# Kernel tuning notes

Hardware: AMD Instinct MI355X
Metric: run time of the kernel (lower is better)

Reference implementation:

```python
import jax, jax.numpy as jnp
import numpy as np

NUM_HEADS = 8
EMBED_DIM = 512
EXPAND = 3
RPE_DIM = 512
RPE_LAYERS = 3
B, N = 4, 2048
D1 = (EXPAND * EMBED_DIM) // NUM_HEADS * NUM_HEADS  # 1536
HEAD_DIM = D1 // NUM_HEADS  # 192


def srms(x):
    # SimpleRMSNorm: x / (||x||_2 * d^{-1/2} + eps)
    d = x.shape[-1]
    rms = jnp.linalg.norm(x, axis=-1, keepdims=True) * (d ** -0.5)
    return x / (rms + 1e-8)


def rpe_net(idx, Wp, bp, Wl, bl, Wr, br):
    # idx: (m, 1) relative positions -> (m, h*head_dim)
    h = idx @ Wp.T + bp
    for i in range(Wl.shape[0]):  # fixed small layer count
        h = jax.nn.relu(srms(h)) @ Wl[i].T + bl[i]
    return jax.nn.relu(srms(h)) @ Wr.T + br


def setup_inputs() -> dict:
    key = jax.random.key(0)
    ks = jax.random.split(key, 12)
    s = 0.02
    return {
        "x": jax.random.normal(ks[0], (B, N, EMBED_DIM), jnp.float32),
        "Wu": jax.random.normal(ks[1], (D1, EMBED_DIM), jnp.float32) * s,
        "bu": jnp.zeros((D1,), jnp.float32),
        "Wv": jax.random.normal(ks[2], (D1, EMBED_DIM), jnp.float32) * s,
        "bv": jnp.zeros((D1,), jnp.float32),
        "Wo": jax.random.normal(ks[3], (EMBED_DIM, D1), jnp.float32) * s,
        "bo": jnp.zeros((EMBED_DIM,), jnp.float32),
        "Wp": jax.random.normal(ks[4], (RPE_DIM, 1), jnp.float32) * s,
        "bp": jax.random.normal(ks[5], (RPE_DIM,), jnp.float32) * s,
        "Wl": jax.random.normal(ks[6], (RPE_LAYERS, RPE_DIM, RPE_DIM), jnp.float32) * s,
        "bl": jax.random.normal(ks[7], (RPE_LAYERS, RPE_DIM), jnp.float32) * s,
        "Wr": jax.random.normal(ks[8], (NUM_HEADS * HEAD_DIM, RPE_DIM), jnp.float32) * s,
        "br": jax.random.normal(ks[9], (NUM_HEADS * HEAD_DIM,), jnp.float32) * s,
    }


def reference(x, Wu, bu, Wv, bv, Wo, bo, Wp, bp, Wl, bl, Wr, br):
    b, n, e = x.shape
    d1 = Wu.shape[0]
    hd = d1 // NUM_HEADS
    u = jax.nn.silu(x @ Wu.T + bu)                       # (b, n, d1)
    v = jax.nn.silu(x @ Wv.T + bv)                       # (b, n, d1)
    v = v.reshape(b, n, NUM_HEADS, hd).transpose(0, 2, 1, 3)  # (b, h, n, d)
    # Tno non-causal, par_type=1: indices [0, 1..n-1, 0, -(n-1)..-1]
    pos = jnp.arange(1, n, dtype=x.dtype)
    zero = jnp.zeros((1,), x.dtype)
    idx = jnp.concatenate([zero, pos, zero, -pos[::-1]])[:, None]  # (2n, 1)
    a = rpe_net(idx, Wp, bp, Wl, bl, Wr, br)             # (2n, h*d)
    a = a.reshape(2 * n, NUM_HEADS, hd).transpose(1, 0, 2)  # (h, 2n, d)
    m = 2 * n
    # circular conv of length 2n along sequence, truncate to n
    y = jnp.fft.rfft(v, m, axis=2) * jnp.fft.rfft(a, m, axis=1)[None]
    out = jnp.fft.irfft(y, m, axis=2)[:, :, :n, :]       # (b, h, n, d)
    out = out.transpose(0, 2, 1, 3).reshape(b, n, d1)    # (b, n, d1)
    return (u * out) @ Wo.T + bo
```

## Files before the change

### kernel.cpp

```cpp
#include <hip/hip_runtime.h>

#define N_SEQ 2048
#define M_FFT 4096
#define D1    1536
#define NH    8
#define HD    192
#define ED    512

typedef __bf16 bf16;
typedef __bf16 bf16x2 __attribute__((ext_vector_type(2)));
typedef __bf16 bf16x4 __attribute__((ext_vector_type(4)));
typedef __bf16 bf16x8 __attribute__((ext_vector_type(8)));
typedef float  floatx4 __attribute__((ext_vector_type(4)));

enum { MODE_PLAIN = 0, MODE_SILU_VT = 2, MODE_AT = 3 };

__device__ __forceinline__ void gload16(const void* g, void* l) {
    __builtin_amdgcn_global_load_lds(
        (const __attribute__((address_space(1))) void*)g,
        (__attribute__((address_space(3))) void*)l, 16, 0, 0);
}

template<int MODE, typename OutT>
__global__ __launch_bounds__(256) void gemm_bf16(
    const bf16* __restrict__ A, const bf16* __restrict__ Bw,
    const float* __restrict__ bias, OutT* __restrict__ C,
    int M, int Nc, int K)
{
    __shared__ __align__(16) bf16 As[128 * 32];
    __shared__ __align__(16) bf16 Bs[128 * 32];

    const int tid  = threadIdx.x;
    const int row0 = blockIdx.y * 128;
    const int col0 = blockIdx.x * 128;
    const int wid  = tid >> 6;
    const int lane = tid & 63;
    const int lm   = lane & 15;
    const int lk   = lane >> 4;
    const int wm   = wid >> 1;
    const int wn   = wid & 1;
    const int ldrow  = tid >> 2;
    const int ldcol8 = (tid & 3) * 8;

    floatx4 acc[4][4] = {};

    const bf16* Ag = A  + ((size_t)(row0 + ldrow)) * K + ldcol8;
    const bf16* Bg = Bw + ((size_t)(col0 + ldrow)) * K + ldcol8;
    bf16* AsW = As + (wid * 16) * 32;
    bf16* BsW = Bs + (wid * 16) * 32;

    for (int k0 = 0; k0 < K; k0 += 32) {
        gload16(Ag + k0, AsW);
        gload16(Ag + (size_t)64 * K + k0, AsW + 64 * 32);
        gload16(Bg + k0, BsW);
        gload16(Bg + (size_t)64 * K + k0, BsW + 64 * 32);
        __syncthreads();

        bf16x8 af[4], bfr[4];
        #pragma unroll
        for (int mi = 0; mi < 4; ++mi)
            af[mi] = *(const bf16x8*)&As[(wm * 64 + mi * 16 + lm) * 32 + lk * 8];
        #pragma unroll
        for (int nj = 0; nj < 4; ++nj)
            bfr[nj] = *(const bf16x8*)&Bs[(wn * 64 + nj * 16 + lm) * 32 + lk * 8];
        #pragma unroll
        for (int mi = 0; mi < 4; ++mi)
            #pragma unroll
            for (int nj = 0; nj < 4; ++nj)
                acc[mi][nj] = __builtin_amdgcn_mfma_f32_16x16x32_bf16(
                    af[mi], bfr[nj], acc[mi][nj], 0, 0, 0);
        __syncthreads();
    }

    float bcol[4];
    #pragma unroll
    for (int nj = 0; nj < 4; ++nj)
        bcol[nj] = bias[col0 + wn * 64 + nj * 16 + lm];

    #pragma unroll
    for (int mi = 0; mi < 4; ++mi) {
        const int rbase = row0 + wm * 64 + mi * 16 + lk * 4;
        #pragma unroll
        for (int nj = 0; nj < 4; ++nj) {
            const int col = col0 + wn * 64 + nj * 16 + lm;
            float vals[4];
            #pragma unroll
            for (int r = 0; r < 4; ++r) {
                float val = acc[mi][nj][r] + bcol[nj];
                if (MODE == MODE_SILU_VT)
                    val = val / (1.0f + __expf(-val));
                vals[r] = val;
            }
            if (MODE == MODE_SILU_VT) {
                int b = rbase >> 11, s = rbase & 2047;
                bf16x4 o;
                #pragma unroll
                for (int r = 0; r < 4; ++r) o[r] = (bf16)vals[r];
                *(bf16x4*)&((bf16*)C)[((size_t)(b * D1 + col)) * N_SEQ + s] = o;
            } else if (MODE == MODE_AT) {
                float4 o = make_float4(vals[0], vals[1], vals[2], vals[3]);
                *(float4*)&((float*)C)[(size_t)col * M + rbase] = o;
            } else {
                #pragma unroll
                for (int r = 0; r < 4; ++r)
                    C[(size_t)(rbase + r) * Nc + col] = (OutT)vals[r];
            }
        }
    }
}

__global__ __launch_bounds__(256) void f2b_kernel(
    const float* __restrict__ in, bf16* __restrict__ out, int n)
{
    int i = (blockIdx.x * 256 + threadIdx.x) * 4;
    if (i >= n) return;
    float4 f = *(const float4*)(in + i);
    union { bf16 h[4]; short4 s; } u4;
    u4.h[0] = (bf16)f.x; u4.h[1] = (bf16)f.y;
    u4.h[2] = (bf16)f.z; u4.h[3] = (bf16)f.w;
    *(short4*)(out + i) = u4.s;
}

__global__ __launch_bounds__(256) void f2b5_kernel(
    const float* __restrict__ s0, const float* __restrict__ s1,
    const float* __restrict__ s2, const float* __restrict__ s3,
    const float* __restrict__ s4, bf16* __restrict__ dst)
{
    const int seg = blockIdx.y;
    const float* src = seg == 0 ? s0 : seg == 1 ? s1 : seg == 2 ? s2
                     : seg == 3 ? s3 : s4;
    int i = (blockIdx.x * 256 + threadIdx.x) * 4;
    float4 f = *(const float4*)(src + i);
    union { bf16 h[4]; short4 s; } u4;
    u4.h[0] = (bf16)f.x; u4.h[1] = (bf16)f.y;
    u4.h[2] = (bf16)f.z; u4.h[3] = (bf16)f.w;
    *(short4*)(dst + (size_t)seg * 786432 + i) = u4.s;
}

__global__ __launch_bounds__(256) void rpe_in_srms_kernel(
    const float* __restrict__ Wp, const float* __restrict__ bp,
    bf16* __restrict__ g)
{
    const int j = blockIdx.x;
    const int tid = threadIdx.x;
    float idxv = (j < N_SEQ) ? (float)j
                             : (j == N_SEQ ? 0.0f : (float)(j - 2 * N_SEQ));
    float h1 = idxv * Wp[tid] + bp[tid];
    float h2 = idxv * Wp[tid + 256] + bp[tid + 256];
    float ss = h1 * h1 + h2 * h2;
    #pragma unroll
    for (int off = 32; off > 0; off >>= 1) ss += __shfl_down(ss, off, 64);
    __shared__ float red[4];
    if ((tid & 63) == 0) red[tid >> 6] = ss;
    __syncthreads();
    float tot = red[0] + red[1] + red[2] + red[3];
    float scale = 1.0f / (sqrtf(tot) * 0.04419417382415922f + 1e-8f);
    g[(size_t)j * ED + tid]       = (bf16)fmaxf(h1 * scale, 0.0f);
    g[(size_t)j * ED + tid + 256] = (bf16)fmaxf(h2 * scale, 0.0f);
}

__global__ __launch_bounds__(256) void srms_relu_kernel(
    const float* __restrict__ in, bf16* __restrict__ out)
{
    const int row = blockIdx.x;
    const int tid = threadIdx.x;
    const float* p = in + (size_t)row * ED;

    float ss = 0.0f;
    for (int i = tid; i < ED; i += 256) { float x = p[i]; ss += x * x; }
    #pragma unroll
    for (int off = 32; off > 0; off >>= 1) ss += __shfl_down(ss, off, 64);
    __shared__ float red[4];
    if ((tid & 63) == 0) red[tid >> 6] = ss;
    __syncthreads();
    float tot = red[0] + red[1] + red[2] + red[3];
    float scale = 1.0f / (sqrtf(tot) * 0.04419417382415922f + 1e-8f);
    for (int i = tid; i < ED; i += 256)
        out[(size_t)row * ED + i] = (bf16)fmaxf(p[i] * scale, 0.0f);
}

#define FFT_LDS_SZ 4381

__device__ __forceinline__ int fpad(int i) { return i + (i >> 4) + 2 * (i >> 8); }

__device__ __forceinline__ float2 cmul(float2 a, float2 b) {
    return make_float2(a.x * b.x - a.y * b.y, a.x * b.y + a.y * b.x);
}
__device__ __forceinline__ float2 cadd(float2 a, float2 b) {
    return make_float2(a.x + b.x, a.y + b.y);
}
__device__ __forceinline__ float2 csub(float2 a, float2 b) {
    return make_float2(a.x - b.x, a.y - b.y);
}
__host__ __device__ constexpr int brev4(int t) {
    return ((t & 1) << 3) | ((t & 2) << 1) | ((t & 4) >> 1) | ((t & 8) >> 3);
}

template<bool FWD>
__device__ __forceinline__ void w16_tab(float2 w[8]) {
    const float sg = FWD ? -1.0f : 1.0f;
    const float C1 = 0.9238795325112867f, S1 = 0.3826834323650898f;
    const float C2 = 0.7071067811865476f;
    w[0] = make_float2( 1.f, 0.f);
    w[1] = make_float2( C1, sg * S1);
    w[2] = make_float2( C2, sg * C2);
    w[3] = make_float2( S1, sg * C1);
    w[4] = make_float2(0.f, sg * 1.f);
    w[5] = make_float2(-S1, sg * C1);
    w[6] = make_float2(-C2, sg * C2);
    w[7] = make_float2(-C1, sg * S1);
}

__device__ __forceinline__ void fft16_dif_tail(float2 x[16], const float2 w[8]) {
    #pragma unroll
    for (int b = 0; b < 16; b += 8)
        #pragma unroll
        for (int k = 0; k < 4; ++k) {
            float2 u = x[b + k], t = x[b + k + 4];
            x[b + k] = cadd(u, t); x[b + k + 4] = cmul(csub(u, t), w[2 * k]);
        }
    #pragma unroll
    for (int b = 0; b < 16; b += 4)
        #pragma unroll
        for (int k = 0; k < 2; ++k) {
            float2 u = x[b + k], t = x[b + k + 2];
            x[b + k] = cadd(u, t); x[b + k + 2] = cmul(csub(u, t), w[4 * k]);
        }
    #pragma unroll
    for (int b = 0; b < 16; b += 2) {
        float2 u = x[b], t = x[b + 1];
        x[b] = cadd(u, t); x[b + 1] = csub(u, t);
    }
}

__device__ __forceinline__ void fft16_dif(float2 x[16]) {
    float2 w[8]; w16_tab<true>(w);
    #pragma unroll
    for (int k = 0; k < 8; ++k) {
        float2 u = x[k], t = x[k + 8];
        x[k] = cadd(u, t); x[k + 8] = cmul(csub(u, t), w[k]);
    }
    fft16_dif_tail(x, w);
}

__device__ __forceinline__ void fft16_dif_halfzero(float2 x[16]) {
    float2 w[8]; w16_tab<true>(w);
    x[8] = x[0];
    #pragma unroll
    for (int k = 1; k < 8; ++k) x[k + 8] = cmul(x[k], w[k]);
    fft16_dif_tail(x, w);
}

template<bool HALF_OUT>
__device__ __forceinline__ void fft16_dit_inv(float2 x[16]) {
    float2 w[8]; w16_tab<false>(w);
    #pragma unroll
    for (int b = 0; b < 16; b += 2) {
        float2 u = x[b], t = x[b + 1];
        x[b] = cadd(u, t); x[b + 1] = csub(u, t);
    }
    #pragma unroll
    for (int b = 0; b < 16; b += 4)
        #pragma unroll
        for (int k = 0; k < 2; ++k) {
            float2 u = x[b + k], t = cmul(x[b + k + 2], w[4 * k]);
            x[b + k] = cadd(u, t); x[b + k + 2] = csub(u, t);
        }
    #pragma unroll
    for (int b = 0; b < 16; b += 8)
        #pragma unroll
        for (int k = 0; k < 4; ++k) {
            float2 u = x[b + k], t = cmul(x[b + k + 4], w[2 * k]);
            x[b + k] = cadd(u, t); x[b + k + 4] = csub(u, t);
        }
    #pragma unroll
    for (int k = 0; k < 8; ++k) {
        float2 u = x[k], t = cmul(x[k + 8], w[k]);
        x[k] = cadd(u, t);
        if (!HALF_OUT) x[k + 8] = csub(u, t);
    }
}

__device__ __forceinline__ void stage_twiddle(float2 v[16], int j, float den, float sgn)
{
    float s, c;
    __sincosf(sgn * 6.283185307179586f * (float)j / den, &s, &c);
    float2 w1 = make_float2(c, s), wt = make_float2(1.f, 0.f);
    #pragma unroll
    for (int tau = 1; tau < 16; ++tau) {
        wt = cmul(wt, w1);
        v[brev4(tau)] = cmul(v[brev4(tau)], wt);
    }
}

template<bool HALF_ZERO>
__device__ void fft4096_fwd(float2* d, int tid)
{
    float2 v[16];
    {
        const int j = tid;
        if (HALF_ZERO) {
            #pragma unroll
            for (int t = 0; t < 8; ++t) v[t] = d[fpad(j + (t << 8))];
            fft16_dif_halfzero(v);
        } else {
            #pragma unroll
            for (int t = 0; t < 16; ++t) v[t] = d[fpad(j + (t << 8))];
            fft16_dif(v);
        }
        stage_twiddle(v, j, 4096.0f, -1.0f);
        #pragma unroll
        for (int p = 0; p < 16; ++p) d[fpad(j + (p << 8))] = v[p];
    }
    __syncthreads();
    {
        const int base = ((tid >> 4) << 8) + (tid & 15);
        #pragma unroll
        for (int t = 0; t < 16; ++t) v[t] = d[fpad(base + (t << 4))];
        fft16_dif(v);
        stage_twiddle(v, tid & 15, 256.0f, -1.0f);
        #pragma unroll
        for (int p = 0; p < 16; ++p) d[fpad(base + (p << 4))] = v[p];
    }
    __syncthreads();
    {
        const int base = tid << 4;
        #pragma unroll
        for (int t = 0; t < 16; ++t) v[t] = d[fpad(base + t)];
        fft16_dif(v);
        #pragma unroll
        for (int p = 0; p < 16; ++p) d[fpad(base + p)] = v[p];
    }
    __syncthreads();
}

template<bool HALF_OUT>
__device__ void fft4096_inv(float2* d, int tid)
{
    float2 v[16];
    {
        const int base = tid << 4;
        #pragma unroll
        for (int p = 0; p < 16; ++p) v[p] = d[fpad(base + p)];
        fft16_dit_inv<false>(v);
        #pragma unroll
        for (int t = 0; t < 16; ++t) d[fpad(base + t)] = v[t];
    }
    __syncthreads();
    {
        const int base = ((tid >> 4) << 8) + (tid & 15);
        #pragma unroll
        for (int p = 0; p < 16; ++p) v[p] = d[fpad(base + (p << 4))];
        stage_twiddle(v, tid & 15, 256.0f, 1.0f);
        fft16_dit_inv<false>(v);
        #pragma unroll
        for (int t = 0; t < 16; ++t) d[fpad(base + (t << 4))] = v[t];
    }
    __syncthreads();
    {
        const int j = tid;
        #pragma unroll
        for (int p = 0; p < 16; ++p) v[p] = d[fpad(j + (p << 8))];
        stage_twiddle(v, j, 4096.0f, 1.0f);
        fft16_dit_inv<HALF_OUT>(v);
        #pragma unroll
        for (int t = 0; t < (HALF_OUT ? 8 : 16); ++t) d[fpad(j + (t << 8))] = v[t];
    }
    __syncthreads();
}

__global__ __launch_bounds__(256) void fft_a_kernel(
    const float* __restrict__ a_t, float2* __restrict__ Wspec)
{
    __shared__ float2 data[FFT_LDS_SZ];
    const int tid = threadIdx.x;
    const int h = blockIdx.x / 96, dp = blockIdx.x % 96;

    const float* r0 = a_t + ((size_t)(h * HD + 2 * dp)) * M_FFT;
    const float* r1 = r0 + M_FFT;

    for (int j = tid; j < 4096; j += 256) data[fpad(j)] = make_float2(r0[j], r1[j]);
    __syncthreads();
    fft4096_fwd<false>(data, tid);

    float2* outrow = Wspec + (size_t)blockIdx.x * 4096;
    for (int j = tid; j < 4096; j += 256) outrow[j] = data[fpad(j)];
}

__global__ __launch_bounds__(256) void fft_conv_kernel(
    const bf16* __restrict__ v_t, const float2* __restrict__ Wspec,
    const bf16* __restrict__ u_t, bf16* __restrict__ gated_t)
{
    __shared__ float2 data[FFT_LDS_SZ];
    const int tid = threadIdx.x;
    const int bx = blockIdx.x;
    const int b  = bx / 768;
    const int r  = bx % 768;
    const int h  = r / 96, dp = r % 96;
    const int ch = h * HD + 2 * dp;

    const bf16* z0 = v_t + ((size_t)(b * D1 + ch)) * N_SEQ;
    const bf16* z1 = z0 + N_SEQ;

    {
        const int s = tid * 8;
        bf16x8 a0 = *(const bf16x8*)(z0 + s);
        bf16x8 a1 = *(const bf16x8*)(z1 + s);
        #pragma unroll
        for (int i = 0; i < 8; ++i)
            data[fpad(s + i)] = make_float2((float)a0[i], (float)a1[i]);
    }
    __syncthreads();

    fft4096_fwd<true>(data, tid);

    const float2* Wrow = Wspec + (size_t)r * 4096;
    for (int k = tid; k <= 2048; k += 256) {
        int km = (4096 - k) & 4095;
        int p1 = __brev((unsigned)k)  >> 20;
        int p2 = __brev((unsigned)km) >> 20;
        float2 Zk = data[fpad(p1)], Zm = data[fpad(p2)];
        float2 Wk = Wrow[p1], Wm = Wrow[p2];
        float2 V0 = make_float2(0.5f * (Zk.x + Zm.x), 0.5f * (Zk.y - Zm.y));
        float2 V1 = make_float2(0.5f * (Zk.y + Zm.y), 0.5f * (Zm.x - Zk.x));
        float2 A0 = make_float2(0.5f * (Wk.x + Wm.x), 0.5f * (Wk.y - Wm.y));
        float2 A1 = make_float2(0.5f * (Wk.y + Wm.y), 0.5f * (Wm.x - Wk.x));
        float2 P = make_float2(V0.x * A0.x - V0.y * A0.y, V0.x * A0.y + V0.y * A0.x);
        float2 Q = make_float2(V1.x * A1.x - V1.y * A1.y, V1.x * A1.y + V1.y * A1.x);
        data[fpad(p1)] = make_float2(P.x - Q.y, P.y + Q.x);
        if (k != 0 && k != 2048)
            data[fpad(p2)] = make_float2(P.x + Q.y, Q.x - P.y);
    }
    __syncthreads();

    fft4096_inv<true>(data, tid);

    const float inv_m = 1.0f / 4096.0f;
    const bf16* u0 = u_t + ((size_t)(b * D1 + ch)) * N_SEQ;
    const bf16* u1 = u0 + N_SEQ;
    bf16* g0 = gated_t + ((size_t)(b * D1 + ch)) * N_SEQ;
    bf16* g1 = g0 + N_SEQ;
    {
        const int t = tid * 8;
        bf16x8 ua = *(const bf16x8*)(u0 + t);
        bf16x8 ub = *(const bf16x8*)(u1 + t);
        bf16x8 oa, ob;
        #pragma unroll
        for (int i = 0; i < 8; ++i) {
            float2 y = data[fpad(t + i)];
            oa[i] = (bf16)(y.x * inv_m * (float)ua[i]);
            ob[i] = (bf16)(y.y * inv_m * (float)ub[i]);
        }
        *(bf16x8*)(g0 + t) = oa;
        *(bf16x8*)(g1 + t) = ob;
    }
}

__global__ __launch_bounds__(256) void transpose_cs_kernel(
    const bf16* __restrict__ in, bf16* __restrict__ outp)
{
    __shared__ bf16 tile[64 * 68];
    const int c0 = blockIdx.x * 64;
    const int m0 = blockIdx.y * 64;
    const int b  = m0 >> 11;
    const int s0 = m0 & 2047;
    const int tid = threadIdx.x;
    const int cl = tid >> 4;
    const int sc = (tid & 15) * 4;
    #pragma unroll
    for (int p = 0; p < 4; ++p) {
        int c = p * 16 + cl;
        bf16x4 v = *(const bf16x4*)&in[((size_t)(b * D1 + c0 + c)) * N_SEQ + s0 + sc];
        *(bf16x4*)&tile[c * 68 + sc] = v;
    }
    __syncthreads();
    const int sl = tid >> 4;
    const int cc = (tid & 15) * 4;
    #pragma unroll
    for (int p = 0; p < 4; ++p) {
        int s = p * 16 + sl;
        bf16x4 o;
        #pragma unroll
        for (int j = 0; j < 4; ++j) o[j] = tile[(cc + j) * 68 + s];
        *(bf16x4*)&outp[((size_t)(m0 + s)) * D1 + c0 + cc] = o;
    }
}

extern "C" void kernel_launch(void* const* d_in, const int* in_sizes, int n_in,
                              void* d_out, int out_size, void* d_ws, size_t ws_size,
                              hipStream_t stream)
{
    const float* x  = (const float*)d_in[0];
    const float* Wu = (const float*)d_in[1];
    const float* bu = (const float*)d_in[2];
    const float* Wv = (const float*)d_in[3];
    const float* bv = (const float*)d_in[4];
    const float* Wo = (const float*)d_in[5];
    const float* bo = (const float*)d_in[6];
    const float* Wp = (const float*)d_in[7];
    const float* bp = (const float*)d_in[8];
    const float* Wl = (const float*)d_in[9];
    const float* bl = (const float*)d_in[10];
    const float* Wr = (const float*)d_in[11];
    const float* br = (const float*)d_in[12];
    float* out = (float*)d_out;

    float* ws      = (float*)d_ws;
    float* a_t     = ws;
    float* Wspec   = a_t   + 6291456;
    float* h0      = Wspec + 6291456;
    bf16*  bfws    = (bf16*)(h0 + 2097152);
    bf16*  x_bf    = bfws;
    bf16*  w_bf    = x_bf    + 4194304;
    bf16*  Wu_bf   = w_bf;
    bf16*  Wv_bf   = Wu_bf   + 786432;
    bf16*  Wo_bf   = Wv_bf   + 786432;
    bf16*  Wl_bf   = Wo_bf   + 786432;
    bf16*  Wr_bf   = Wl_bf   + 786432;
    bf16*  g_bf    = Wr_bf   + 786432;
    bf16*  u_t     = g_bf    + 2097152;
    bf16*  v_t     = u_t     + 12582912;
    bf16*  gated_t = v_t     + 12582912;
    bf16*  gated   = gated_t + 12582912;

    dim3 blk(256);

    f2b_kernel<<<4194304 / 1024, blk, 0, stream>>>(x, x_bf, 4194304);
    f2b5_kernel<<<dim3(786432 / 1024, 5), blk, 0, stream>>>(
        Wu, Wv, Wo, Wl, Wr, w_bf);

    gemm_bf16<MODE_SILU_VT, bf16><<<dim3(12, 64), blk, 0, stream>>>(
        x_bf, Wu_bf, bu, u_t, 8192, D1, ED);
    gemm_bf16<MODE_SILU_VT, bf16><<<dim3(12, 64), blk, 0, stream>>>(
        x_bf, Wv_bf, bv, v_t, 8192, D1, ED);

    rpe_in_srms_kernel<<<4096, blk, 0, stream>>>(Wp, bp, g_bf);
    for (int i = 0; i < 3; ++i) {
        gemm_bf16<MODE_PLAIN, float><<<dim3(4, 32), blk, 0, stream>>>(
            g_bf, Wl_bf + (size_t)i * ED * ED, bl + (size_t)i * ED,
            h0, 4096, ED, ED);
        srms_relu_kernel<<<4096, blk, 0, stream>>>(h0, g_bf);
    }
    gemm_bf16<MODE_AT, float><<<dim3(12, 32), blk, 0, stream>>>(
        g_bf, Wr_bf, br, a_t, 4096, D1, ED);

    fft_a_kernel<<<768, blk, 0, stream>>>(a_t, (float2*)Wspec);
    fft_conv_kernel<<<3072, blk, 0, stream>>>(
        v_t, (const float2*)Wspec, u_t, gated_t);

    transpose_cs_kernel<<<dim3(24, 128), blk, 0, stream>>>(gated_t, gated);

    gemm_bf16<MODE_PLAIN, float><<<dim3(4, 64), blk, 0, stream>>>(
        gated, Wo_bf, bo, out, 8192, ED, D1);
}
```

Baseline: 380.7 us.

## Fuse U/V projection GEMMs and use radix-4 FFT with LDS twiddle table

The separate Wu and Wv projection GEMMs become one launch over concatenated weights, with the epilogue sending each column block to u_t or v_t with its own bias. This relies on Wu and Wv being adjacent in the bf16 weight buffer, and it halves the number of passes over x. The radix-16 FFT butterflies are rewritten as radix-4 decompositions, where trivial twiddles become swaps and sign flips. Per-stage sincos/recurrence twiddles are replaced by lookups into a 2048-entry LDS table built in each block, which costs extra LDS and a small setup loop per block.

```diff
diff --git a/kernel.cpp b/kernel.cpp
--- a/kernel.cpp
+++ b/kernel.cpp
@@ -13,7 +13,7 @@
 typedef __bf16 bf16x8 __attribute__((ext_vector_type(8)));
 typedef float  floatx4 __attribute__((ext_vector_type(4)));
 
-enum { MODE_PLAIN = 0, MODE_SILU_VT = 2, MODE_AT = 3 };
+enum { MODE_PLAIN = 0, MODE_SILU_UV = 1, MODE_AT = 3 };
 
 __device__ __forceinline__ void gload16(const void* g, void* l) {
     __builtin_amdgcn_global_load_lds(
@@ -24,7 +24,8 @@
 template<int MODE, typename OutT>
 __global__ __launch_bounds__(256) void gemm_bf16(
     const bf16* __restrict__ A, const bf16* __restrict__ Bw,
-    const float* __restrict__ bias, OutT* __restrict__ C,
+    const float* __restrict__ bias, const float* __restrict__ bias2,
+    OutT* __restrict__ C, OutT* __restrict__ C2,
     int M, int Nc, int K)
 {
     __shared__ __align__(16) bf16 As[128 * 32];
@@ -72,31 +73,36 @@
         __syncthreads();
     }
 
+    const float* bs = bias;
+    OutT* dst = C;
+    int cadj = 0;
+    if (MODE == MODE_SILU_UV && col0 >= D1) { bs = bias2; dst = C2; cadj = D1; }
+
     float bcol[4];
     #pragma unroll
     for (int nj = 0; nj < 4; ++nj)
-        bcol[nj] = bias[col0 + wn * 64 + nj * 16 + lm];
+        bcol[nj] = bs[col0 - cadj + wn * 64 + nj * 16 + lm];
 
     #pragma unroll
     for (int mi = 0; mi < 4; ++mi) {
         const int rbase = row0 + wm * 64 + mi * 16 + lk * 4;
         #pragma unroll
         for (int nj = 0; nj < 4; ++nj) {
-            const int col = col0 + wn * 64 + nj * 16 + lm;
+            const int col = col0 - cadj + wn * 64 + nj * 16 + lm;
             float vals[4];
             #pragma unroll
             for (int r = 0; r < 4; ++r) {
                 float val = acc[mi][nj][r] + bcol[nj];
-                if (MODE == MODE_SILU_VT)
+                if (MODE == MODE_SILU_UV)
                     val = val / (1.0f + __expf(-val));
                 vals[r] = val;
             }
-            if (MODE == MODE_SILU_VT) {
+            if (MODE == MODE_SILU_UV) {
                 int b = rbase >> 11, s = rbase & 2047;
                 bf16x4 o;
                 #pragma unroll
                 for (int r = 0; r < 4; ++r) o[r] = (bf16)vals[r];
-                *(bf16x4*)&((bf16*)C)[((size_t)(b * D1 + col)) * N_SEQ + s] = o;
+                *(bf16x4*)&((bf16*)dst)[((size_t)(b * D1 + col)) * N_SEQ + s] = o;
             } else if (MODE == MODE_AT) {
                 float4 o = make_float4(vals[0], vals[1], vals[2], vals[3]);
                 *(float4*)&((float*)C)[(size_t)col * M + rbase] = o;
@@ -180,6 +186,9 @@
 }
 
 #define FFT_LDS_SZ 4381
+#define CC1 0.9238795325112867f
+#define SS1 0.3826834323650898f
+#define RR2 0.7071067811865476f
 
 __device__ __forceinline__ int fpad(int i) { return i + (i >> 4) + 2 * (i >> 8); }
 
@@ -192,109 +201,116 @@
 __device__ __forceinline__ float2 csub(float2 a, float2 b) {
     return make_float2(a.x - b.x, a.y - b.y);
 }
+__device__ __forceinline__ float2 cneg_i(float2 a) { return make_float2(a.y, -a.x); }
+__device__ __forceinline__ float2 cpos_i(float2 a) { return make_float2(-a.y, a.x); }
 __host__ __device__ constexpr int brev4(int t) {
     return ((t & 1) << 3) | ((t & 2) << 1) | ((t & 4) >> 1) | ((t & 8) >> 3);
 }
 
-template<bool FWD>
-__device__ __forceinline__ void w16_tab(float2 w[8]) {
-    const float sg = FWD ? -1.0f : 1.0f;
-    const float C1 = 0.9238795325112867f, S1 = 0.3826834323650898f;
-    const float C2 = 0.7071067811865476f;
-    w[0] = make_float2( 1.f, 0.f);
-    w[1] = make_float2( C1, sg * S1);
-    w[2] = make_float2( C2, sg * C2);
-    w[3] = make_float2( S1, sg * C1);
-    w[4] = make_float2(0.f, sg * 1.f);
-    w[5] = make_float2(-S1, sg * C1);
-    w[6] = make_float2(-C2, sg * C2);
-    w[7] = make_float2(-C1, sg * S1);
-}
-
-__device__ __forceinline__ void fft16_dif_tail(float2 x[16], const float2 w[8]) {
-    #pragma unroll
-    for (int b = 0; b < 16; b += 8)
-        #pragma unroll
-        for (int k = 0; k < 4; ++k) {
-            float2 u = x[b + k], t = x[b + k + 4];
-            x[b + k] = cadd(u, t); x[b + k + 4] = cmul(csub(u, t), w[2 * k]);
+template<bool HZ>
+__device__ __forceinline__ void fft16_dif_r4(float2 x[16]) {
+    const float2 W1 = make_float2( CC1, -SS1);
+    const float2 W2 = make_float2( RR2, -RR2);
+    const float2 W3 = make_float2( SS1, -CC1);
+    const float2 W6 = make_float2(-RR2, -RR2);
+    const float2 W9 = make_float2(-CC1,  SS1);
+    #pragma unroll
+    for (int n = 0; n < 4; ++n) {
+        float2 A, B, C, D;
+        if (HZ) { A = x[n]; C = x[n]; B = x[n + 4]; D = x[n + 4]; }
+        else {
+            A = cadd(x[n], x[n + 8]);  C = csub(x[n], x[n + 8]);
+            B = cadd(x[n + 4], x[n + 12]); D = csub(x[n + 4], x[n + 12]);
         }
-    #pragma unroll
-    for (int b = 0; b < 16; b += 4)
-        #pragma unroll
-        for (int k = 0; k < 2; ++k) {
-            float2 u = x[b + k], t = x[b + k + 2];
-            x[b + k] = cadd(u, t); x[b + k + 2] = cmul(csub(u, t), w[4 * k]);
+        float2 s = csub(A, B);
+        float2 nid = cneg_i(D);
+        float2 m = cadd(C, nid);
+        float2 p = csub(C, nid);
+        x[n] = cadd(A, B);
+        if (n == 0)      { x[4] = s;            x[8]  = m;           x[12] = p; }
+        else if (n == 1) { x[5] = cmul(s, W2);  x[9]  = cmul(m, W1); x[13] = cmul(p, W3); }
+        else if (n == 2) { x[6] = cneg_i(s);    x[10] = cmul(m, W2); x[14] = cmul(p, W6); }
+        else             { x[7] = cmul(s, W6);  x[11] = cmul(m, W3); x[15] = cmul(p, W9); }
+    }
+    #pragma unroll
+    for (int q = 0; q < 16; q += 4) {
+        float2 a = x[q], b = x[q + 1], c = x[q + 2], d = x[q + 3];
+        float2 a1 = cadd(a, c), c1 = csub(a, c);
+        float2 b1 = cadd(b, d), d1 = cneg_i(csub(b, d));
+        x[q]     = cadd(a1, b1);
+        x[q + 1] = csub(a1, b1);
+        x[q + 2] = cadd(c1, d1);
+        x[q + 3] = csub(c1, d1);
+    }
+}
+
+template<bool HALF_OUT>
+__device__ __forceinline__ void fft16_dit_inv_r4(float2 x[16]) {
+    const float2 V1 = make_float2( CC1, SS1);
+    const float2 V2 = make_float2( RR2, RR2);
+    const float2 V3 = make_float2( SS1, CC1);
+    const float2 V6 = make_float2(-RR2, RR2);
+    #pragma unroll
+    for (int q = 0; q < 16; q += 4) {
+        float2 a = x[q], b = x[q + 1], c = x[q + 2], d = x[q + 3];
+        float2 a1 = cadd(a, b), b1 = csub(a, b);
+        float2 c1 = cadd(c, d), d1 = csub(c, d);
+        float2 t = cpos_i(d1);
+        x[q]     = cadd(a1, c1);
+        x[q + 2] = csub(a1, c1);
+        x[q + 1] = cadd(b1, t);
+        x[q + 3] = csub(b1, t);
+    }
+    #pragma unroll
+    for (int n = 0; n < 4; ++n) {
+        float2 t1, t2;
+        if (n == 0)      { t1 = x[4];             t2 = x[12]; }
+        else if (n == 1) { t1 = cmul(x[5],  V2);  t2 = cmul(x[13], V2); }
+        else if (n == 2) { t1 = cpos_i(x[6]);     t2 = cpos_i(x[14]); }
+        else             { t1 = cmul(x[7],  V6);  t2 = cmul(x[15], V6); }
+        float2 P = cadd(x[n], t1), Q = csub(x[n], t1);
+        float2 R = cadd(x[n + 8], t2), S = csub(x[n + 8], t2);
+        float2 t, u;
+        if (n == 0)      { t = R;            u = S; }
+        else if (n == 1) { t = cmul(R, V1);  u = cmul(S, V1); }
+        else if (n == 2) { t = cmul(R, V2);  u = cmul(S, V2); }
+        else             { t = cmul(R, V3);  u = cmul(S, V3); }
+        float2 iu = cpos_i(u);
+        x[n]     = cadd(P, t);
+        x[n + 4] = cadd(Q, iu);
+        if (!HALF_OUT) {
+            x[n + 8]  = csub(P, t);
+            x[n + 12] = csub(Q, iu);
         }
-    #pragma unroll
-    for (int b = 0; b < 16; b += 2) {
-        float2 u = x[b], t = x[b + 1];
-        x[b] = cadd(u, t); x[b + 1] = csub(u, t);
-    }
-}
-
-__device__ __forceinline__ void fft16_dif(float2 x[16]) {
-    float2 w[8]; w16_tab<true>(w);
-    #pragma unroll
-    for (int k = 0; k < 8; ++k) {
-        float2 u = x[k], t = x[k + 8];
-        x[k] = cadd(u, t); x[k + 8] = cmul(csub(u, t), w[k]);
-    }
-    fft16_dif_tail(x, w);
-}
-
-__device__ __forceinline__ void fft16_dif_halfzero(float2 x[16]) {
-    float2 w[8]; w16_tab<true>(w);
-    x[8] = x[0];
-    #pragma unroll
-    for (int k = 1; k < 8; ++k) x[k + 8] = cmul(x[k], w[k]);
-    fft16_dif_tail(x, w);
-}
-
-template<bool HALF_OUT>
-__device__ __forceinline__ void fft16_dit_inv(float2 x[16]) {
-    float2 w[8]; w16_tab<false>(w);
-    #pragma unroll
-    for (int b = 0; b < 16; b += 2) {
-        float2 u = x[b], t = x[b + 1];
-        x[b] = cadd(u, t); x[b + 1] = csub(u, t);
-    }
-    #pragma unroll
-    for (int b = 0; b < 16; b += 4)
-        #pragma unroll
-        for (int k = 0; k < 2; ++k) {
-            float2 u = x[b + k], t = cmul(x[b + k + 2], w[4 * k]);
-            x[b + k] = cadd(u, t); x[b + k + 2] = csub(u, t);
-        }
-    #pragma unroll
-    for (int b = 0; b < 16; b += 8)
-        #pragma unroll
-        for (int k = 0; k < 4; ++k) {
-            float2 u = x[b + k], t = cmul(x[b + k + 4], w[2 * k]);
-            x[b + k] = cadd(u, t); x[b + k + 4] = csub(u, t);
-        }
-    #pragma unroll
-    for (int k = 0; k < 8; ++k) {
-        float2 u = x[k], t = cmul(x[k + 8], w[k]);
-        x[k] = cadd(u, t);
-        if (!HALF_OUT) x[k + 8] = csub(u, t);
-    }
-}
-
-__device__ __forceinline__ void stage_twiddle(float2 v[16], int j, float den, float sgn)
-{
-    float s, c;
-    __sincosf(sgn * 6.283185307179586f * (float)j / den, &s, &c);
-    float2 w1 = make_float2(c, s), wt = make_float2(1.f, 0.f);
+    }
+}
+
+__device__ __forceinline__ void build_twl(float2* twl, int tid)
+{
+    for (int k = tid; k < 2048; k += 256) {
+        float sn, cs;
+        __sincosf(-6.283185307179586f * (float)k * (1.0f / 4096.0f), &sn, &cs);
+        twl[k] = make_float2(cs, sn);
+    }
+}
+
+template<bool CONJ>
+__device__ __forceinline__ void stage_twiddle_tab(
+    float2 v[16], const float2* __restrict__ twl, int j, int mult)
+{
     #pragma unroll
     for (int tau = 1; tau < 16; ++tau) {
-        wt = cmul(wt, w1);
-        v[brev4(tau)] = cmul(v[brev4(tau)], wt);
+        int m = j * tau * mult;
+        float2 t = twl[m & 2047];
+        float sg = (m & 2048) ? -1.0f : 1.0f;
+        t.x *= sg;
+        t.y = CONJ ? -t.y * sg : t.y * sg;
+        v[brev4(tau)] = cmul(v[brev4(tau)], t);
     }
 }
 
 template<bool HALF_ZERO>
-__device__ void fft4096_fwd(float2* d, int tid)
+__device__ void fft4096_fwd(float2* d, const float2* twl, int tid)
 {
     float2 v[16];
     {
@@ -302,13 +318,13 @@
         if (HALF_ZERO) {
             #pragma unroll
             for (int t = 0; t < 8; ++t) v[t] = d[fpad(j + (t << 8))];
-            fft16_dif_halfzero(v);
+            fft16_dif_r4<true>(v);
         } else {
             #pragma unroll
             for (int t = 0; t < 16; ++t) v[t] = d[fpad(j + (t << 8))];
-            fft16_dif(v);
+            fft16_dif_r4<false>(v);
         }
-        stage_twiddle(v, j, 4096.0f, -1.0f);
+        stage_twiddle_tab<false>(v, twl, j, 1);
         #pragma unroll
         for (int p = 0; p < 16; ++p) d[fpad(j + (p << 8))] = v[p];
     }
@@ -317,8 +333,8 @@
         const int base = ((tid >> 4) << 8) + (tid & 15);
         #pragma unroll
         for (int t = 0; t < 16; ++t) v[t] = d[fpad(base + (t << 4))];
-        fft16_dif(v);
-        stage_twiddle(v, tid & 15, 256.0f, -1.0f);
+        fft16_dif_r4<false>(v);
+        stage_twiddle_tab<false>(v, twl, tid & 15, 16);
         #pragma unroll
         for (int p = 0; p < 16; ++p) d[fpad(base + (p << 4))] = v[p];
     }
@@ -327,7 +343,7 @@
         const int base = tid << 4;
         #pragma unroll
         for (int t = 0; t < 16; ++t) v[t] = d[fpad(base + t)];
-        fft16_dif(v);
+        fft16_dif_r4<false>(v);
         #pragma unroll
         for (int p = 0; p < 16; ++p) d[fpad(base + p)] = v[p];
     }
@@ -335,14 +351,14 @@
 }
 
 template<bool HALF_OUT>
-__device__ void fft4096_inv(float2* d, int tid)
+__device__ void fft4096_inv(float2* d, const float2* twl, int tid)
 {
     float2 v[16];
     {
         const int base = tid << 4;
         #pragma unroll
         for (int p = 0; p < 16; ++p) v[p] = d[fpad(base + p)];
-        fft16_dit_inv<false>(v);
+        fft16_dit_inv_r4<false>(v);
         #pragma unroll
         for (int t = 0; t < 16; ++t) d[fpad(base + t)] = v[t];
     }
@@ -351,8 +367,8 @@
         const int base = ((tid >> 4) << 8) + (tid & 15);
         #pragma unroll
         for (int p = 0; p < 16; ++p) v[p] = d[fpad(base + (p << 4))];
-        stage_twiddle(v, tid & 15, 256.0f, 1.0f);
-        fft16_dit_inv<false>(v);
+        stage_twiddle_tab<true>(v, twl, tid & 15, 16);
+        fft16_dit_inv_r4<false>(v);
         #pragma unroll
         for (int t = 0; t < 16; ++t) d[fpad(base + (t << 4))] = v[t];
     }
@@ -361,8 +377,8 @@
         const int j = tid;
         #pragma unroll
         for (int p = 0; p < 16; ++p) v[p] = d[fpad(j + (p << 8))];
-        stage_twiddle(v, j, 4096.0f, 1.0f);
-        fft16_dit_inv<HALF_OUT>(v);
+        stage_twiddle_tab<true>(v, twl, j, 1);
+        fft16_dit_inv_r4<HALF_OUT>(v);
         #pragma unroll
         for (int t = 0; t < (HALF_OUT ? 8 : 16); ++t) d[fpad(j + (t << 8))] = v[t];
     }
@@ -373,15 +389,17 @@
     const float* __restrict__ a_t, float2* __restrict__ Wspec)
 {
     __shared__ float2 data[FFT_LDS_SZ];
+    __shared__ float2 twl[2048];
     const int tid = threadIdx.x;
     const int h = blockIdx.x / 96, dp = blockIdx.x % 96;
 
     const float* r0 = a_t + ((size_t)(h * HD + 2 * dp)) * M_FFT;
     const float* r1 = r0 + M_FFT;
 
+    build_twl(twl, tid);
     for (int j = tid; j < 4096; j += 256) data[fpad(j)] = make_float2(r0[j], r1[j]);
     __syncthreads();
-    fft4096_fwd<false>(data, tid);
+    fft4096_fwd<false>(data, twl, tid);
 
     float2* outrow = Wspec + (size_t)blockIdx.x * 4096;
     for (int j = tid; j < 4096; j += 256) outrow[j] = data[fpad(j)];
@@ -392,6 +410,7 @@
     const bf16* __restrict__ u_t, bf16* __restrict__ gated_t)
 {
     __shared__ float2 data[FFT_LDS_SZ];
+    __shared__ float2 twl[2048];
     const int tid = threadIdx.x;
     const int bx = blockIdx.x;
     const int b  = bx / 768;
@@ -402,6 +421,7 @@
     const bf16* z0 = v_t + ((size_t)(b * D1 + ch)) * N_SEQ;
     const bf16* z1 = z0 + N_SEQ;
 
+    build_twl(twl, tid);
     {
         const int s = tid * 8;
         bf16x8 a0 = *(const bf16x8*)(z0 + s);
@@ -412,7 +432,7 @@
     }
     __syncthreads();
 
-    fft4096_fwd<true>(data, tid);
+    fft4096_fwd<true>(data, twl, tid);
 
     const float2* Wrow = Wspec + (size_t)r * 4096;
     for (int k = tid; k <= 2048; k += 256) {
@@ -433,7 +453,7 @@
     }
     __syncthreads();
 
-    fft4096_inv<true>(data, tid);
+    fft4096_inv<true>(data, twl, tid);
 
     const float inv_m = 1.0f / 4096.0f;
     const bf16* u0 = u_t + ((size_t)(b * D1 + ch)) * N_SEQ;
@@ -512,9 +532,8 @@
     bf16*  bfws    = (bf16*)(h0 + 2097152);
     bf16*  x_bf    = bfws;
     bf16*  w_bf    = x_bf    + 4194304;
-    bf16*  Wu_bf   = w_bf;
-    bf16*  Wv_bf   = Wu_bf   + 786432;
-    bf16*  Wo_bf   = Wv_bf   + 786432;
+    bf16*  Wuv_bf  = w_bf;
+    bf16*  Wo_bf   = w_bf    + 2 * 786432;
     bf16*  Wl_bf   = Wo_bf   + 786432;
     bf16*  Wr_bf   = Wl_bf   + 786432;
     bf16*  g_bf    = Wr_bf   + 786432;
@@ -529,20 +548,18 @@
     f2b5_kernel<<<dim3(786432 / 1024, 5), blk, 0, stream>>>(
         Wu, Wv, Wo, Wl, Wr, w_bf);
 
-    gemm_bf16<MODE_SILU_VT, bf16><<<dim3(12, 64), blk, 0, stream>>>(
-        x_bf, Wu_bf, bu, u_t, 8192, D1, ED);
-    gemm_bf16<MODE_SILU_VT, bf16><<<dim3(12, 64), blk, 0, stream>>>(
-        x_bf, Wv_bf, bv, v_t, 8192, D1, ED);
+    gemm_bf16<MODE_SILU_UV, bf16><<<dim3(24, 64), blk, 0, stream>>>(
+        x_bf, Wuv_bf, bu, bv, u_t, v_t, 8192, 2 * D1, ED);
 
     rpe_in_srms_kernel<<<4096, blk, 0, stream>>>(Wp, bp, g_bf);
     for (int i = 0; i < 3; ++i) {
         gemm_bf16<MODE_PLAIN, float><<<dim3(4, 32), blk, 0, stream>>>(
-            g_bf, Wl_bf + (size_t)i * ED * ED, bl + (size_t)i * ED,
-            h0, 4096, ED, ED);
+            g_bf, Wl_bf + (size_t)i * ED * ED, bl + (size_t)i * ED, nullptr,
+            h0, nullptr, 4096, ED, ED);
         srms_relu_kernel<<<4096, blk, 0, stream>>>(h0, g_bf);
     }
     gemm_bf16<MODE_AT, float><<<dim3(12, 32), blk, 0, stream>>>(
-        g_bf, Wr_bf, br, a_t, 4096, D1, ED);
+        g_bf, Wr_bf, br, nullptr, a_t, nullptr, 4096, D1, ED);
 
     fft_a_kernel<<<768, blk, 0, stream>>>(a_t, (float2*)Wspec);
     fft_conv_kernel<<<3072, blk, 0, stream>>>(
@@ -551,5 +568,5 @@
     transpose_cs_kernel<<<dim3(24, 128), blk, 0, stream>>>(gated_t, gated);
 
     gemm_bf16<MODE_PLAIN, float><<<dim3(4, 64), blk, 0, stream>>>(
-        gated, Wo_bf, bo, out, 8192, ED, D1);
-}
+        gated, Wo_bf, bo, nullptr, out, nullptr, 8192, ED, D1);
+}
```

Measured after the change: 378.3 us. Within noise of the previous version (-0.6%).
